# Kernel tuning notes

Measured on AMD Instinct MI355X. Metric: run time of the kernel, lower is better.

## Reference

```python
import jax, jax.numpy as jnp
import numpy as np

H = 64          # hiddens_dims
K = 3           # Chebyshev order
B = 16          # graphs in batch
NPG = 16384     # nodes per graph
N = B * NPG     # total nodes
E = 2_097_152   # total edges
R = 2191        # num_residues (hard-coded in source)
E_REF = R * 16
HALF = N // 2   # backbone count == sidechain count (mask is balanced per graph)


def _lin(k, fan_in, shape):
    return jax.random.uniform(k, shape, jnp.float32, -1.0, 1.0) / np.sqrt(fan_in)


def setup_inputs() -> dict:
    key = jax.random.key(0)
    ks = jax.random.split(key, 40)
    inp = {}
    inp["x"] = jax.random.normal(ks[0], (N, 3), jnp.float32)
    inp["edge_index"] = jax.random.randint(ks[1], (2, E), 0, N)
    inp["batch"] = jnp.repeat(jnp.arange(B, dtype=jnp.int32), NPG)
    blk = jnp.concatenate([jnp.ones((NPG // 2,), bool), jnp.zeros((NPG // 2,), bool)])
    inp["mask"] = jnp.tile(blk, B)  # backbone=True first half of each graph block
    inp["x_ref"] = jax.random.normal(ks[2], (R, 3), jnp.float32)
    inp["edgeref"] = jax.random.randint(ks[3], (2, E_REF), 0, R)
    i = 4
    for name, cin in [("cw0", 3), ("cw1", H), ("cw2", H), ("rw0", 3), ("rw1", H), ("rw2", H)]:
        inp[name] = _lin(ks[i], cin, (K, cin, H)); i += 1
        inp[name.replace("w", "b")] = jnp.zeros((H,), jnp.float32)  # ChebConv bias init = zeros
    for name, cin, cout in [("mlp_w", 2 * H, H), ("mlpP2_w", 2 * H, H),
                            ("rep0_w", H, H), ("rep1_w", H, H), ("rep2_w", H, 3)]:
        inp[name] = _lin(ks[i], cin, (cin, cout)); i += 1
        inp[name.replace("_w", "_b")] = _lin(ks[i], cin, (cout,)); i += 1
    return inp


def cheb_conv(x, edge_index, W, b, n):
    # PyG ChebConv with sym normalization, lambda_max=2: L_hat = -D^-1/2 A D^-1/2 (diag = 0)
    row, col = edge_index[0], edge_index[1]
    deg = jax.ops.segment_sum(jnp.ones_like(x[:, 0])[row] * 0 + 1.0, row, num_segments=n)
    dinv = jnp.where(deg > 0, jax.lax.rsqrt(jnp.maximum(deg, 1e-12)), 0.0)
    w = -(dinv[row] * dinv[col])  # [E]

    def prop(h):  # L_hat @ h via gather + segment_sum
        return jax.ops.segment_sum(w[:, None] * h[col], row, num_segments=n)

    Tx0 = x
    out = Tx0 @ W[0]
    Tx1 = prop(x)
    out = out + Tx1 @ W[1]
    for k in range(2, K):
        Tx2 = 2.0 * prop(Tx1) - Tx0
        out = out + Tx2 @ W[k]
        Tx0, Tx1 = Tx1, Tx2
    return out + b


def _forward(x, edge_index, mask, x_ref, edgeref,
             cw0, cb0, cw1, cb1, cw2, cb2, rw0, rb0, rw1, rb1, rw2, rb2,
             mlp_w, mlp_b, mlpP2_w, mlpP2_b,
             rep0_w, rep0_b, rep1_w, rep1_b, rep2_w, rep2_b):
    # main GNN stack (tanh after all but last; dropout is identity in eval)
    h = jnp.tanh(cheb_conv(x, edge_index, cw0, cb0, N))
    h = jnp.tanh(cheb_conv(h, edge_index, cw1, cb1, N))
    h = cheb_conv(h, edge_index, cw2, cb2, N)

    bb_idx = jnp.nonzero(mask, size=HALF)[0]
    sc_idx = jnp.nonzero(~mask, size=HALF)[0]
    x_bb = h[bb_idx].reshape(B, -1, H).mean(axis=1)[:, None, :]  # [B,1,H]
    x_sc = h[sc_idx].reshape(B, -1, H).mean(axis=1)[:, None, :]  # [B,1,H]

    # reference-graph stack: source bug makes `conv2 != self.convs[-1]` always True,
    # so tanh follows every convRef layer
    r = jnp.tanh(cheb_conv(x_ref, edgeref, rw0, rb0, R))
    r = jnp.tanh(cheb_conv(r, edgeref, rw1, rb1, R))
    r = jnp.tanh(cheb_conv(r, edgeref, rw2, rb2, R))
    r = jnp.broadcast_to(r[None], (B, R, H))

    bb_rep = jnp.broadcast_to(x_bb, (B, R, H))
    phase1 = jnp.concatenate([r, bb_rep], axis=-1) @ mlp_w + mlp_b        # [B,R,H]
    sc_rep = jnp.broadcast_to(x_sc, (B, R, H))
    phase2 = jnp.concatenate([phase1, sc_rep], axis=-1) @ mlpP2_w + mlpP2_b  # [B,R,H]

    res = phase2.reshape(-1, H)
    res = jax.nn.relu(res @ rep0_w + rep0_b)
    res = jax.nn.relu(res @ rep1_w + rep1_b)
    res = jax.nn.relu(res @ rep2_w + rep2_b)  # [B*R, 3]
    return res.reshape(-1, 3), x_bb, x_sc


def reference(x, edge_index, batch, mask, x_ref, edgeref,
              cw0, cb0, cw1, cb1, cw2, cb2, rw0, rb0, rw1, rb1, rw2, rb2,
              mlp_w, mlp_b, mlpP2_w, mlpP2_b,
              rep0_w, rep0_b, rep1_w, rep1_b, rep2_w, rep2_b):
    del batch  # only used for len(batch.unique()) == B, a static constant here
    return _forward(x, edge_index, mask, x_ref, edgeref,
                    cw0, cb0, cw1, cb1, cw2, cb2, rw0, rb0, rw1, rb1, rw2, rb2,
                    mlp_w, mlp_b, mlpP2_w, mlpP2_b,
                    rep0_w, rep0_b, rep1_w, rep1_b, rep2_w, rep2_b)
```

## Files before the change

### kernel.cpp

```cpp
#include <hip/hip_runtime.h>
#include <hip/hip_fp16.h>
#include <math.h>

#define NN 262144
#define NE 2097152
#define RR 2191
#define ER (RR*16)
#define NB 16
#define BRR (NB*RR)
#define OUT_RES (BRR*3)

typedef __attribute__((ext_vector_type(8))) _Float16 half8;
typedef __attribute__((ext_vector_type(4))) float f32x4;

__global__ void k_hist(const int* __restrict__ row, int* __restrict__ deg, int nE){
  int i = blockIdx.x*blockDim.x + threadIdx.x;
  int st = gridDim.x*blockDim.x;
  for (; i < nE; i += st) atomicAdd(&deg[row[i]], 1);
}

__global__ void k_scan1(const int* __restrict__ deg, int* __restrict__ rowptr,
                        int* __restrict__ partials, float* __restrict__ dinv){
  __shared__ int s[256];
  int t = threadIdx.x; int i = blockIdx.x*256 + t;
  int v = deg[i]; s[t] = v; __syncthreads();
  dinv[i] = v > 0 ? 1.0f/sqrtf((float)v) : 0.0f;
  for (int off = 1; off < 256; off <<= 1){
    int x = (t >= off) ? s[t-off] : 0; __syncthreads();
    s[t] += x; __syncthreads();
  }
  rowptr[i] = s[t] - v;
  if (t == 255) partials[blockIdx.x] = s[255];
}

__global__ void k_scan2(int* __restrict__ partials){
  __shared__ int s[1024];
  int t = threadIdx.x; int v = partials[t]; s[t] = v; __syncthreads();
  for (int off = 1; off < 1024; off <<= 1){
    int x = (t >= off) ? s[t-off] : 0; __syncthreads();
    s[t] += x; __syncthreads();
  }
  partials[t] = s[t] - v;
}

__global__ void k_scan3(int* __restrict__ rowptr, const int* __restrict__ partials){
  int t = threadIdx.x; int i = blockIdx.x*256 + t;
  rowptr[i] += partials[blockIdx.x];
  if (i == 0) rowptr[NN] = NE;
}

__global__ void k_scan_small(const int* __restrict__ deg, int* __restrict__ rowptr,
                             float* __restrict__ dinv, int n){
  __shared__ int s[256];
  int t = threadIdx.x;
  int carry = 0;
  for (int base = 0; base < n; base += 256){
    int idx = base + t;
    int v = (idx < n) ? deg[idx] : 0;
    if (idx < n) dinv[idx] = v > 0 ? 1.0f/sqrtf((float)v) : 0.0f;
    s[t] = v; __syncthreads();
    for (int off = 1; off < 256; off <<= 1){
      int x = (t >= off) ? s[t-off] : 0; __syncthreads();
      s[t] += x; __syncthreads();
    }
    if (idx < n) rowptr[idx] = carry + s[t] - v;
    carry += s[255];
    __syncthreads();
  }
  if (t == 0) rowptr[n] = carry;
}

__global__ void k_scatter(const int* __restrict__ row, const int* __restrict__ col,
                          const float* __restrict__ dinv, const int* __restrict__ rowptr,
                          int* __restrict__ cursor, int2* __restrict__ pair, int nE){
  int i = blockIdx.x*blockDim.x + threadIdx.x;
  int st = gridDim.x*blockDim.x;
  for (; i < nE; i += st){
    int r = row[i], c = col[i];
    int pos = rowptr[r] + atomicAdd(&cursor[r], 1);
    pair[pos] = make_int2(c, __float_as_int(-dinv[r]*dinv[c]));
  }
}

__global__ void k_pad3(const float* __restrict__ src, float4* __restrict__ dst, int n){
  int i = blockIdx.x*blockDim.x + threadIdx.x;
  if (i < n) dst[i] = make_float4(src[i*3], src[i*3+1], src[i*3+2], 0.0f);
}

__global__ void k_prop3p(const float4* __restrict__ h, float4* __restrict__ y,
                         const int* __restrict__ rowptr, const int2* __restrict__ pair, int n){
  int i = blockIdx.x*blockDim.x + threadIdx.x;
  if (i >= n) return;
  float a0 = 0.f, a1 = 0.f, a2 = 0.f;
  int s = rowptr[i], e = rowptr[i+1];
  int p = s;
  for (; p + 4 <= e; p += 4){
    int2 q0 = pair[p], q1 = pair[p+1], q2 = pair[p+2], q3 = pair[p+3];
    float4 v0 = h[q0.x], v1 = h[q1.x], v2 = h[q2.x], v3 = h[q3.x];
    float w0 = __int_as_float(q0.y), w1 = __int_as_float(q1.y);
    float w2 = __int_as_float(q2.y), w3 = __int_as_float(q3.y);
    a0 = fmaf(w0,v0.x, fmaf(w1,v1.x, fmaf(w2,v2.x, fmaf(w3,v3.x, a0))));
    a1 = fmaf(w0,v0.y, fmaf(w1,v1.y, fmaf(w2,v2.y, fmaf(w3,v3.y, a1))));
    a2 = fmaf(w0,v0.z, fmaf(w1,v1.z, fmaf(w2,v2.z, fmaf(w3,v3.z, a2))));
  }
  for (; p < e; p++){
    int2 q = pair[p]; float wv = __int_as_float(q.y);
    float4 v = h[q.x];
    a0 = fmaf(wv, v.x, a0); a1 = fmaf(wv, v.y, a1); a2 = fmaf(wv, v.z, a2);
  }
  y[i] = make_float4(a0, a1, a2, 0.0f);
}

__global__ void k_prop64(const float* __restrict__ h, float* __restrict__ y,
                         const int* __restrict__ rowptr, const int2* __restrict__ pair, int n){
  int t = threadIdx.x, lane = t & 63;
  int i = blockIdx.x*4 + (t >> 6);
  if (i >= n) return;
  float acc = 0.f;
  int s = rowptr[i], e = rowptr[i+1];
  int p = s;
  for (; p + 4 <= e; p += 4){
    int2 q0 = pair[p], q1 = pair[p+1], q2 = pair[p+2], q3 = pair[p+3];
    float v0 = h[(size_t)q0.x*64 + lane], v1 = h[(size_t)q1.x*64 + lane];
    float v2 = h[(size_t)q2.x*64 + lane], v3 = h[(size_t)q3.x*64 + lane];
    acc = fmaf(__int_as_float(q0.y),v0, fmaf(__int_as_float(q1.y),v1,
          fmaf(__int_as_float(q2.y),v2, fmaf(__int_as_float(q3.y),v3, acc))));
  }
  for (; p < e; p++){
    int2 q = pair[p];
    acc = fmaf(__int_as_float(q.y), h[(size_t)q.x*64 + lane], acc);
  }
  y[(size_t)i*64 + lane] = acc;
}

__global__ void __launch_bounds__(256) k_prop64h(
    const uint4* __restrict__ h4, uint4* __restrict__ y4,
    const int* __restrict__ rowptr, const int2* __restrict__ pair, int n){
  int t = threadIdx.x;
  int sub = t & 7;
  int row = blockIdx.x*32 + (t >> 3);
  if (row >= n) return;
  int s = rowptr[row], e = rowptr[row+1];
  float ac[8];
  #pragma unroll
  for (int k = 0; k < 8; k++) ac[k] = 0.f;
  int p = s;
  for (; p + 8 <= e; p += 8){
    int2 q[8]; uint4 v[8];
    #pragma unroll
    for (int j = 0; j < 8; j++) q[j] = pair[p+j];
    #pragma unroll
    for (int j = 0; j < 8; j++) v[j] = h4[(size_t)q[j].x*8 + sub];
    #pragma unroll
    for (int j = 0; j < 8; j++){
      float wv = __int_as_float(q[j].y);
      #pragma unroll
      for (int k = 0; k < 4; k++){
        float2 f = __half22float2(((const __half2*)&v[j])[k]);
        ac[2*k]   = fmaf(wv, f.x, ac[2*k]);
        ac[2*k+1] = fmaf(wv, f.y, ac[2*k+1]);
      }
    }
  }
  for (; p + 4 <= e; p += 4){
    int2 q[4]; uint4 v[4];
    #pragma unroll
    for (int j = 0; j < 4; j++) q[j] = pair[p+j];
    #pragma unroll
    for (int j = 0; j < 4; j++) v[j] = h4[(size_t)q[j].x*8 + sub];
    #pragma unroll
    for (int j = 0; j < 4; j++){
      float wv = __int_as_float(q[j].y);
      #pragma unroll
      for (int k = 0; k < 4; k++){
        float2 f = __half22float2(((const __half2*)&v[j])[k]);
        ac[2*k]   = fmaf(wv, f.x, ac[2*k]);
        ac[2*k+1] = fmaf(wv, f.y, ac[2*k+1]);
      }
    }
  }
  for (; p < e; p++){
    int2 q = pair[p];
    float wv = __int_as_float(q.y);
    uint4 v = h4[(size_t)q.x*8 + sub];
    #pragma unroll
    for (int k = 0; k < 4; k++){
      float2 f = __half22float2(((const __half2*)&v)[k]);
      ac[2*k]   = fmaf(wv, f.x, ac[2*k]);
      ac[2*k+1] = fmaf(wv, f.y, ac[2*k+1]);
    }
  }
  uint4 r;
  #pragma unroll
  for (int k = 0; k < 4; k++){
    __half2 hp = __floats2half2_rn(ac[2*k], ac[2*k+1]);
    ((unsigned*)&r)[k] = *(unsigned*)&hp;
  }
  y4[(size_t)row*8 + sub] = r;
}

__global__ void k_combine3f(const float4* __restrict__ x, const float4* __restrict__ t1,
                            const float4* __restrict__ t2, const float* __restrict__ W,
                            const float* __restrict__ bias, float* __restrict__ out, int n){
  int t = threadIdx.x, lane = t & 63;
  int i = blockIdx.x*4 + (t >> 6);
  if (i >= n) return;
  float4 px = x[i], p1 = t1[i], p2 = t2[i];
  const float* fx = (const float*)&px;
  const float* f1 = (const float*)&p1;
  const float* f2 = (const float*)&p2;
  float acc = bias[lane];
  #pragma unroll
  for (int j = 0; j < 3; j++){
    float x0 = fx[j], x1 = f1[j];
    float x2 = 2.0f*f2[j] - x0;
    acc += x0*W[      j*64 + lane]
         + x1*W[192 + j*64 + lane]
         + x2*W[384 + j*64 + lane];
  }
  out[(size_t)i*64 + lane] = tanhf(acc);
}

__global__ void k_combine3h(const float4* __restrict__ x, const float4* __restrict__ t1,
                            const float4* __restrict__ t2, const float* __restrict__ W,
                            const float* __restrict__ bias, __half* __restrict__ out, int n){
  int t = threadIdx.x, lane = t & 63;
  int i = blockIdx.x*4 + (t >> 6);
  if (i >= n) return;
  float4 px = x[i], p1 = t1[i], p2 = t2[i];
  const float* fx = (const float*)&px;
  const float* f1 = (const float*)&p1;
  const float* f2 = (const float*)&p2;
  float acc = bias[lane];
  #pragma unroll
  for (int j = 0; j < 3; j++){
    float x0 = fx[j], x1 = f1[j];
    float x2 = 2.0f*f2[j] - x0;
    acc += x0*W[      j*64 + lane]
         + x1*W[192 + j*64 + lane]
         + x2*W[384 + j*64 + lane];
  }
  out[(size_t)i*64 + lane] = __float2half_rn(tanhf(acc));
}

__global__ void k_weff(const float* __restrict__ W, float* __restrict__ D){
  int i = blockIdx.x*blockDim.x + threadIdx.x;
  D[i]        = W[i] - W[8192 + i];
  D[4096 + i] = W[4096 + i];
  D[8192 + i] = 2.0f * W[8192 + i];
}

__global__ void k_wpack(const float* __restrict__ W, _Float16* __restrict__ D){
  int t = blockIdx.x*blockDim.x + threadIdx.x;
  int reg = t & 7, lane = (t >> 3) & 63, nt = (t >> 9) & 3, kc = t >> 11;
  int m = kc >> 1;
  int kin = (kc & 1)*32 + ((lane >> 4) & 3)*8 + reg;
  int n = nt*16 + (lane & 15);
  float eff;
  if      (m == 0) eff = W[kin*64 + n] - W[8192 + kin*64 + n];
  else if (m == 1) eff = W[4096 + kin*64 + n];
  else             eff = 2.0f * W[8192 + kin*64 + n];
  D[t] = (_Float16)eff;
}

__global__ void __launch_bounds__(256) k_combine64m(
    const __half* A, const __half* B, const __half* C,
    const _Float16* __restrict__ wfrag, const float* __restrict__ bias,
    __half* out, int ntiles, int wavestride){
  int t = threadIdx.x;
  int lane = t & 63;
  int wv = blockIdx.x*4 + (t >> 6);
  half8 bf[24];
  #pragma unroll
  for (int i = 0; i < 24; i++)
    bf[i] = *(const half8*)(wfrag + ((size_t)(i*64 + lane))*8);
  int col = lane & 15, grp = (lane >> 4) & 3;
  float b0 = bias[col], b1 = bias[16+col], b2 = bias[32+col], b3 = bias[48+col];
  for (int tile = wv; tile < ntiles; tile += wavestride){
    size_t rb = (size_t)tile*16;
    f32x4 acc0 = {b0,b0,b0,b0}, acc1 = {b1,b1,b1,b1};
    f32x4 acc2 = {b2,b2,b2,b2}, acc3 = {b3,b3,b3,b3};
    #pragma unroll
    for (int kc = 0; kc < 6; kc++){
      const __half* s = (kc < 2) ? A : (kc < 4) ? B : C;
      half8 a = *(const half8*)(s + (rb + col)*64 + (kc & 1)*32 + grp*8);
      acc0 = __builtin_amdgcn_mfma_f32_16x16x32_f16(a, bf[kc*4+0], acc0, 0,0,0);
      acc1 = __builtin_amdgcn_mfma_f32_16x16x32_f16(a, bf[kc*4+1], acc1, 0,0,0);
      acc2 = __builtin_amdgcn_mfma_f32_16x16x32_f16(a, bf[kc*4+2], acc2, 0,0,0);
      acc3 = __builtin_amdgcn_mfma_f32_16x16x32_f16(a, bf[kc*4+3], acc3, 0,0,0);
    }
    __half* o = out + (rb + grp*4)*64;
    #pragma unroll
    for (int r = 0; r < 4; r++){
      o[(size_t)r*64 +      col] = __float2half_rn(tanhf(acc0[r]));
      o[(size_t)r*64 + 16 + col] = __float2half_rn(tanhf(acc1[r]));
      o[(size_t)r*64 + 32 + col] = __float2half_rn(tanhf(acc2[r]));
      o[(size_t)r*64 + 48 + col] = __float2half_rn(tanhf(acc3[r]));
    }
  }
}

__global__ void k_pool3(const __half2* __restrict__ hA, const __half2* __restrict__ hB,
                        const __half2* __restrict__ hC, float* __restrict__ pA,
                        float* __restrict__ pB, float* __restrict__ pC){
  const __half2* src = (blockIdx.y == 0) ? hA : (blockIdx.y == 1) ? hB : hC;
  float* dst         = (blockIdx.y == 0) ? pA : (blockIdx.y == 1) ? pB : pC;
  int blk = blockIdx.x;
  int chunk = blk & 15, seg = blk >> 4;
  int t = threadIdx.x, ch2 = t & 31, rsub = t >> 5;
  int base = seg*8192 + chunk*512;
  float ax = 0.f, ay = 0.f;
  for (int j = 0; j < 64; j++){
    int row = base + rsub + j*8;
    float2 v = __half22float2(src[(size_t)row*32 + ch2]);
    ax += v.x; ay += v.y;
  }
  __shared__ float sx[256], sy[256];
  sx[t] = ax; sy[t] = ay; __syncthreads();
  if (t < 32){
    float tx = 0.f, ty = 0.f;
    #pragma unroll
    for (int j = 0; j < 8; j++){ tx += sx[ch2 + j*32]; ty += sy[ch2 + j*32]; }
    int b = seg >> 1, half_ = seg & 1;
    atomicAdd(&dst[half_*1024 + b*64 + ch2*2],     tx);
    atomicAdd(&dst[half_*1024 + b*64 + ch2*2 + 1], ty);
  }
}

__global__ void k_combine_pooled(const float* __restrict__ pA, const float* __restrict__ pB,
                                 const float* __restrict__ pC, const float* __restrict__ weff,
                                 const float* __restrict__ bias, float* __restrict__ xbbsc,
                                 float* __restrict__ dout){
  int i = blockIdx.x*blockDim.x + threadIdx.x;
  int pr = i >> 6, c = i & 63;
  const float* a = pA + pr*64;
  const float* b = pB + pr*64;
  const float* cc = pC + pr*64;
  float v = 0.f;
  for (int k = 0; k < 64; k++){
    v = fmaf(a[k],  weff[        k*64 + c], v);
    v = fmaf(b[k],  weff[4096 +  k*64 + c], v);
    v = fmaf(cc[k], weff[8192 +  k*64 + c], v);
  }
  v = v*(1.0f/8192.0f) + bias[c];
  xbbsc[i] = v;
  dout[OUT_RES + i] = v;
}

__global__ void __launch_bounds__(256) k_combine64f(
    const float* __restrict__ A, const float* __restrict__ Bm, const float* __restrict__ C,
    const float* __restrict__ Weff, const float* __restrict__ bias,
    float* __restrict__ out, int n){
  int t = threadIdx.x;
  int lane = t & 63;
  int wid  = __builtin_amdgcn_readfirstlane(t >> 6);
  int half_ = wid & 1;
  int row  = blockIdx.x*128 + (wid >> 1)*64 + lane;
  bool active = (row < n);
  float acc[32];
  #pragma unroll
  for (int c = 0; c < 32; c++) acc[c] = bias[half_*32 + c];
  if (active){
    #pragma unroll 1
    for (int m = 0; m < 3; m++){
      const float* src = (m == 0 ? A : (m == 1 ? Bm : C)) + (size_t)row*64;
      const float* Wm  = Weff + m*4096 + half_*32;
      #pragma unroll 1
      for (int k4 = 0; k4 < 16; k4++){
        float4 a4 = *(const float4*)(src + k4*4);
        const float* wk = Wm + k4*256;
        #pragma unroll
        for (int kk = 0; kk < 4; kk++){
          float a = (kk == 0) ? a4.x : (kk == 1) ? a4.y : (kk == 2) ? a4.z : a4.w;
          #pragma unroll
          for (int c = 0; c < 32; c++)
            acc[c] = fmaf(a, wk[kk*64 + c], acc[c]);
        }
      }
    }
  }
  __syncthreads();
  if (active){
    float* o = out + (size_t)row*64 + half_*32;
    #pragma unroll
    for (int c = 0; c < 32; c++) o[c] = tanhf(acc[c]);
  }
}

__global__ void k_refchain(const float* __restrict__ refA, const float* __restrict__ mlp_w,
                           const float* __restrict__ mlp2_w, const float* __restrict__ rep0_w,
                           float* __restrict__ rt3a, int n){
  int t = threadIdx.x, lane = t & 63;
  int i = blockIdx.x*4 + (t >> 6);
  if (i >= n) return;
  float v = refA[i*64 + lane];
  float a = 0.f;
  #pragma unroll
  for (int k = 0; k < 64; k++) a += __shfl(v, k, 64) * mlp_w[k*64 + lane];
  float b = 0.f;
  #pragma unroll
  for (int k = 0; k < 64; k++) b += __shfl(a, k, 64) * mlp2_w[k*64 + lane];
  float c = 0.f;
  #pragma unroll
  for (int k = 0; k < 64; k++) c += __shfl(b, k, 64) * rep0_w[k*64 + lane];
  rt3a[i*64 + lane] = c;
}

__global__ void k_bbchain(const float* __restrict__ xbbsc,
                          const float* __restrict__ mlp_w,  const float* __restrict__ mlp_b,
                          const float* __restrict__ mlp2_w, const float* __restrict__ mlp2_b,
                          const float* __restrict__ rep0_w, const float* __restrict__ rep0_b,
                          float* __restrict__ bt3a){
  int t = threadIdx.x, lane = t & 63;
  int i = blockIdx.x*4 + (t >> 6);
  if (i >= NB) return;
  float vbb = xbbsc[i*64 + lane];
  float vsc = xbbsc[1024 + i*64 + lane];
  float a = mlp_b[lane];
  #pragma unroll
  for (int k = 0; k < 64; k++) a += __shfl(vbb, k, 64) * mlp_w[4096 + k*64 + lane];
  float b = mlp2_b[lane];
  #pragma unroll
  for (int k = 0; k < 64; k++) b += __shfl(a, k, 64) * mlp2_w[k*64 + lane];
  #pragma unroll
  for (int k = 0; k < 64; k++) b += __shfl(vsc, k, 64) * mlp2_w[4096 + k*64 + lane];
  float c = rep0_b[lane];
  #pragma unroll
  for (int k = 0; k < 64; k++) c += __shfl(b, k, 64) * rep0_w[k*64 + lane];
  bt3a[i*64 + lane] = c;
}

__global__ void k_final(const float* __restrict__ rt3, const float* __restrict__ bt3,
                        const float* __restrict__ W1, const float* __restrict__ b1,
                        const float* __restrict__ W2, const float* __restrict__ b2,
                        float* __restrict__ dout){
  int t = threadIdx.x, lane = t & 63;
  int g = blockIdx.x*4 + (t >> 6);
  if (g >= BRR) return;
  int b = g / RR, r = g - b*RR;
  float m = rt3[r*64 + lane] + bt3[b*64 + lane];
  m = fmaxf(m, 0.0f);
  float acc = b1[lane];
  #pragma unroll
  for (int k = 0; k < 64; k++) acc += __shfl(m, k, 64) * W1[k*64 + lane];
  float u = fmaxf(acc, 0.0f);
  float p0 = u*W2[lane*3+0], p1 = u*W2[lane*3+1], p2 = u*W2[lane*3+2];
  #pragma unroll
  for (int off = 32; off > 0; off >>= 1){
    p0 += __shfl_xor(p0, off, 64);
    p1 += __shfl_xor(p1, off, 64);
    p2 += __shfl_xor(p2, off, 64);
  }
  if (lane == 0){
    dout[g*3+0] = fmaxf(p0 + b2[0], 0.0f);
    dout[g*3+1] = fmaxf(p1 + b2[1], 0.0f);
    dout[g*3+2] = fmaxf(p2 + b2[2], 0.0f);
  }
}

extern "C" void kernel_launch(void* const* d_in, const int* in_sizes, int n_in,
                              void* d_out, int out_size, void* d_ws, size_t ws_size,
                              hipStream_t stream){
  const float* x     = (const float*)d_in[0];
  const int*   eidx  = (const int*)d_in[1];
  const float* x_ref = (const float*)d_in[4];
  const int*   eref  = (const int*)d_in[5];
  const float* cw0 = (const float*)d_in[6],  *cb0 = (const float*)d_in[7];
  const float* cw1 = (const float*)d_in[8],  *cb1 = (const float*)d_in[9];
  const float* cw2 = (const float*)d_in[10], *cb2 = (const float*)d_in[11];
  const float* rw0 = (const float*)d_in[12], *rb0 = (const float*)d_in[13];
  const float* rw1 = (const float*)d_in[14], *rb1 = (const float*)d_in[15];
  const float* rw2 = (const float*)d_in[16], *rb2 = (const float*)d_in[17];
  const float* mlp_w  = (const float*)d_in[18], *mlp_b  = (const float*)d_in[19];
  const float* mlp2_w = (const float*)d_in[20], *mlp2_b = (const float*)d_in[21];
  const float* rep0_w = (const float*)d_in[22], *rep0_b = (const float*)d_in[23];
  const float* rep1_w = (const float*)d_in[24], *rep1_b = (const float*)d_in[25];
  const float* rep2_w = (const float*)d_in[26], *rep2_b = (const float*)d_in[27];
  float* out = (float*)d_out;

  char* w = (char*)d_ws;
  size_t off = 0;
  auto alloc = [&](size_t bytes)->void*{
    void* p = w + off;
    off = (off + bytes + 255) & ~(size_t)255;
    return p;
  };
  int*   deg     = (int*)  alloc(NN*4);
  int*   cursor  = (int*)  alloc(NN*4);
  int*   degR    = (int*)  alloc(RR*4);
  int*   cursorR = (int*)  alloc(RR*4);
  float* poolA   = (float*)alloc(2048*4);
  float* poolB   = (float*)alloc(2048*4);
  float* poolC   = (float*)alloc(2048*4);
  size_t zero_bytes = off;

  int*   rowptr   = (int*)  alloc((NN+1)*4);
  int*   partials = (int*)  alloc(1024*4);
  int*   rowptrR  = (int*)  alloc((RR+1)*4);
  float* dinv     = (float*)alloc(NN*4);
  float* dinvR    = (float*)alloc(RR*4);
  int2*  cpair    = (int2*) alloc((size_t)NE*8);
  int2*  cpairR   = (int2*) alloc((size_t)ER*8);
  float4* x4      = (float4*)alloc((size_t)NN*16);
  float4* t1_4    = (float4*)alloc((size_t)NN*16);
  float4* t2_4    = (float4*)alloc((size_t)NN*16);
  float4* xr4     = (float4*)alloc((size_t)RR*16);
  float4* rt1_4   = (float4*)alloc((size_t)RR*16);
  float4* rt2_4   = (float4*)alloc((size_t)RR*16);
  __half* hA      = (__half*)alloc((size_t)NN*64*2);
  __half* hB      = (__half*)alloc((size_t)NN*64*2);
  __half* hC      = (__half*)alloc((size_t)NN*64*2);
  float* refA     = (float*)alloc(RR*64*4);
  float* refB     = (float*)alloc(RR*64*4);
  float* refC     = (float*)alloc(RR*64*4);
  float* xbbsc    = (float*)alloc(2048*4);
  float* rt3a     = (float*)alloc(RR*64*4);
  float* bt3a     = (float*)alloc(NB*64*4);
  float* weffC2   = (float*)alloc(12288*4);
  float* weffR1   = (float*)alloc(12288*4);
  float* weffR2   = (float*)alloc(12288*4);
  _Float16* wfragC1 = (_Float16*)alloc(12288*2);
  (void)ws_size; (void)in_sizes; (void)n_in; (void)out_size;

  hipMemsetAsync(d_ws, 0, zero_bytes, stream);

  k_weff<<<16, 256, 0, stream>>>(cw2, weffC2);
  k_weff<<<16, 256, 0, stream>>>(rw1, weffR1);
  k_weff<<<16, 256, 0, stream>>>(rw2, weffR2);
  k_wpack<<<48, 256, 0, stream>>>(cw1, wfragC1);
  k_pad3<<<1024, 256, 0, stream>>>(x, x4, NN);
  k_pad3<<<9, 256, 0, stream>>>(x_ref, xr4, RR);

  k_hist<<<2048, 256, 0, stream>>>(eidx, deg, NE);
  k_hist<<<64,   256, 0, stream>>>(eref, degR, ER);
  k_scan1<<<1024, 256, 0, stream>>>(deg, rowptr, partials, dinv);
  k_scan2<<<1, 1024, 0, stream>>>(partials);
  k_scan3<<<1024, 256, 0, stream>>>(rowptr, partials);
  k_scan_small<<<1, 256, 0, stream>>>(degR, rowptrR, dinvR, RR);
  k_scatter<<<2048, 256, 0, stream>>>(eidx, eidx+NE, dinv, rowptr, cursor, cpair, NE);
  k_scatter<<<64,   256, 0, stream>>>(eref, eref+ER, dinvR, rowptrR, cursorR, cpairR, ER);

  k_prop3p<<<1024, 256, 0, stream>>>(x4, t1_4, rowptr, cpair, NN);
  k_prop3p<<<1024, 256, 0, stream>>>(t1_4, t2_4, rowptr, cpair, NN);
  k_combine3h<<<NN/4, 256, 0, stream>>>(x4, t1_4, t2_4, cw0, cb0, hA, NN);
  k_prop64h<<<NN/32, 256, 0, stream>>>((const uint4*)hA, (uint4*)hB, rowptr, cpair, NN);
  k_prop64h<<<NN/32, 256, 0, stream>>>((const uint4*)hB, (uint4*)hC, rowptr, cpair, NN);
  k_combine64m<<<1024, 256, 0, stream>>>(hA, hB, hC, wfragC1, cb1, hA, NN/16, 4096);
  k_prop64h<<<NN/32, 256, 0, stream>>>((const uint4*)hA, (uint4*)hB, rowptr, cpair, NN);
  k_prop64h<<<NN/32, 256, 0, stream>>>((const uint4*)hB, (uint4*)hC, rowptr, cpair, NN);
  k_pool3<<<dim3(512,3), 256, 0, stream>>>((const __half2*)hA, (const __half2*)hB,
                                           (const __half2*)hC, poolA, poolB, poolC);
  k_combine_pooled<<<8, 256, 0, stream>>>(poolA, poolB, poolC, weffC2, cb2, xbbsc, out);

  k_prop3p<<<9, 256, 0, stream>>>(xr4, rt1_4, rowptrR, cpairR, RR);
  k_prop3p<<<9, 256, 0, stream>>>(rt1_4, rt2_4, rowptrR, cpairR, RR);
  k_combine3f<<<548, 256, 0, stream>>>(xr4, rt1_4, rt2_4, rw0, rb0, refA, RR);
  k_prop64<<<548, 256, 0, stream>>>(refA, refB, rowptrR, cpairR, RR);
  k_prop64<<<548, 256, 0, stream>>>(refB, refC, rowptrR, cpairR, RR);
  k_combine64f<<<(RR+127)/128, 256, 0, stream>>>(refA, refB, refC, weffR1, rb1, refA, RR);
  k_prop64<<<548, 256, 0, stream>>>(refA, refB, rowptrR, cpairR, RR);
  k_prop64<<<548, 256, 0, stream>>>(refB, refC, rowptrR, cpairR, RR);
  k_combine64f<<<(RR+127)/128, 256, 0, stream>>>(refA, refB, refC, weffR2, rb2, refA, RR);

  k_refchain<<<548, 256, 0, stream>>>(refA, mlp_w, mlp2_w, rep0_w, rt3a, RR);
  k_bbchain<<<4, 256, 0, stream>>>(xbbsc, mlp_w, mlp_b, mlp2_w, mlp2_b, rep0_w, rep0_b, bt3a);

  k_final<<<(BRR+3)/4, 256, 0, stream>>>(rt3a, bt3a, rep1_w, rep1_b, rep2_w, rep2_b, out);
}
```

Measured before the change: 769.9 us.

## Record per-edge rank during histogram and fuse preprocessing kernels into fewer launches

The histogram pass now stores each edge's atomic return value as a byte rank, so the CSR scatter computes its slot as rowptr plus rank and no longer needs a second atomic pass over a cursor array. The main-graph and reference-graph histogram, scan and scatter kernels are merged into shared launches, and the six weight and padding prep kernels become one 2D-grid kernel. The scatter also uses nontemporal stores. This cuts launch count and atomic traffic, but it assumes every node degree fits in a byte, adds a rank buffer write and read, and the edge order within a row now follows histogram atomic order.

```diff
diff --git a/kernel.cpp b/kernel.cpp
--- a/kernel.cpp
+++ b/kernel.cpp
@@ -13,10 +13,22 @@
 typedef __attribute__((ext_vector_type(8))) _Float16 half8;
 typedef __attribute__((ext_vector_type(4))) float f32x4;
 
-__global__ void k_hist(const int* __restrict__ row, int* __restrict__ deg, int nE){
-  int i = blockIdx.x*blockDim.x + threadIdx.x;
-  int st = gridDim.x*blockDim.x;
-  for (; i < nE; i += st) atomicAdd(&deg[row[i]], 1);
+__global__ void k_hist2(const int* __restrict__ eM, int* __restrict__ degM,
+                        unsigned char* __restrict__ rankM,
+                        const int* __restrict__ eR, int* __restrict__ degR,
+                        unsigned char* __restrict__ rankR){
+  int b = blockIdx.x;
+  if (b < 2048){
+    for (int i = b*256 + threadIdx.x; i < NE; i += 2048*256){
+      int old = atomicAdd(&degM[eM[i]], 1);
+      rankM[i] = (unsigned char)old;
+    }
+  } else {
+    for (int i = (b-2048)*256 + threadIdx.x; i < ER; i += 64*256){
+      int old = atomicAdd(&degR[eR[i]], 1);
+      rankR[i] = (unsigned char)old;
+    }
+  }
 }
 
 __global__ void k_scan1(const int* __restrict__ deg, int* __restrict__ rowptr,
@@ -33,14 +45,36 @@
   if (t == 255) partials[blockIdx.x] = s[255];
 }
 
-__global__ void k_scan2(int* __restrict__ partials){
+__global__ void __launch_bounds__(1024) k_scan2m(int* __restrict__ partials,
+                                                 const int* __restrict__ degR,
+                                                 int* __restrict__ rowptrR,
+                                                 float* __restrict__ dinvR){
   __shared__ int s[1024];
-  int t = threadIdx.x; int v = partials[t]; s[t] = v; __syncthreads();
-  for (int off = 1; off < 1024; off <<= 1){
-    int x = (t >= off) ? s[t-off] : 0; __syncthreads();
-    s[t] += x; __syncthreads();
-  }
-  partials[t] = s[t] - v;
+  int t = threadIdx.x;
+  if (blockIdx.x == 0){
+    int v = partials[t]; s[t] = v; __syncthreads();
+    for (int off = 1; off < 1024; off <<= 1){
+      int x = (t >= off) ? s[t-off] : 0; __syncthreads();
+      s[t] += x; __syncthreads();
+    }
+    partials[t] = s[t] - v;
+  } else {
+    int carry = 0;
+    for (int base = 0; base < RR; base += 1024){
+      int idx = base + t;
+      int v = (idx < RR) ? degR[idx] : 0;
+      if (idx < RR) dinvR[idx] = v > 0 ? 1.0f/sqrtf((float)v) : 0.0f;
+      s[t] = v; __syncthreads();
+      for (int off = 1; off < 1024; off <<= 1){
+        int x = (t >= off) ? s[t-off] : 0; __syncthreads();
+        s[t] += x; __syncthreads();
+      }
+      if (idx < RR) rowptrR[idx] = carry + s[t] - v;
+      carry += s[1023];
+      __syncthreads();
+    }
+    if (t == 0) rowptrR[RR] = carry;
+  }
 }
 
 __global__ void k_scan3(int* __restrict__ rowptr, const int* __restrict__ partials){
@@ -49,42 +83,65 @@
   if (i == 0) rowptr[NN] = NE;
 }
 
-__global__ void k_scan_small(const int* __restrict__ deg, int* __restrict__ rowptr,
-                             float* __restrict__ dinv, int n){
-  __shared__ int s[256];
-  int t = threadIdx.x;
-  int carry = 0;
-  for (int base = 0; base < n; base += 256){
-    int idx = base + t;
-    int v = (idx < n) ? deg[idx] : 0;
-    if (idx < n) dinv[idx] = v > 0 ? 1.0f/sqrtf((float)v) : 0.0f;
-    s[t] = v; __syncthreads();
-    for (int off = 1; off < 256; off <<= 1){
-      int x = (t >= off) ? s[t-off] : 0; __syncthreads();
-      s[t] += x; __syncthreads();
-    }
-    if (idx < n) rowptr[idx] = carry + s[t] - v;
-    carry += s[255];
-    __syncthreads();
-  }
-  if (t == 0) rowptr[n] = carry;
-}
-
-__global__ void k_scatter(const int* __restrict__ row, const int* __restrict__ col,
-                          const float* __restrict__ dinv, const int* __restrict__ rowptr,
-                          int* __restrict__ cursor, int2* __restrict__ pair, int nE){
+__global__ void k_scatter2(const int* __restrict__ eM, const float* __restrict__ dinv,
+                           const int* __restrict__ rowptr, const unsigned char* __restrict__ rankM,
+                           int2* __restrict__ pair,
+                           const int* __restrict__ eR, const float* __restrict__ dinvR,
+                           const int* __restrict__ rowptrR, const unsigned char* __restrict__ rankR,
+                           int2* __restrict__ pairR){
+  int b = blockIdx.x;
+  if (b < 2048){
+    for (int i = b*256 + threadIdx.x; i < NE; i += 2048*256){
+      int r = eM[i], c = eM[NE + i];
+      int pos = rowptr[r] + rankM[i];
+      unsigned wbits = (unsigned)__float_as_int(-dinv[r]*dinv[c]);
+      long long v = (unsigned)c | ((long long)wbits << 32);
+      __builtin_nontemporal_store(v, (long long*)(pair + pos));
+    }
+  } else {
+    for (int i = (b-2048)*256 + threadIdx.x; i < ER; i += 64*256){
+      int r = eR[i], c = eR[ER + i];
+      int pos = rowptrR[r] + rankR[i];
+      unsigned wbits = (unsigned)__float_as_int(-dinvR[r]*dinvR[c]);
+      long long v = (unsigned)c | ((long long)wbits << 32);
+      __builtin_nontemporal_store(v, (long long*)(pairR + pos));
+    }
+  }
+}
+
+__global__ void k_prep(const float* __restrict__ cw1, const float* __restrict__ cw2,
+                       const float* __restrict__ rw1, const float* __restrict__ rw2,
+                       float* __restrict__ weffC2, float* __restrict__ weffR1,
+                       float* __restrict__ weffR2, _Float16* __restrict__ wfragC1,
+                       const float* __restrict__ x, float4* __restrict__ x4,
+                       const float* __restrict__ x_ref, float4* __restrict__ xr4){
+  int y = blockIdx.y;
   int i = blockIdx.x*blockDim.x + threadIdx.x;
-  int st = gridDim.x*blockDim.x;
-  for (; i < nE; i += st){
-    int r = row[i], c = col[i];
-    int pos = rowptr[r] + atomicAdd(&cursor[r], 1);
-    pair[pos] = make_int2(c, __float_as_int(-dinv[r]*dinv[c]));
-  }
-}
-
-__global__ void k_pad3(const float* __restrict__ src, float4* __restrict__ dst, int n){
-  int i = blockIdx.x*blockDim.x + threadIdx.x;
-  if (i < n) dst[i] = make_float4(src[i*3], src[i*3+1], src[i*3+2], 0.0f);
+  if (y < 3){
+    if (i < 4096){
+      const float* W = (y == 0) ? cw2 : (y == 1) ? rw1 : rw2;
+      float* D       = (y == 0) ? weffC2 : (y == 1) ? weffR1 : weffR2;
+      D[i]        = W[i] - W[8192 + i];
+      D[4096 + i] = W[4096 + i];
+      D[8192 + i] = 2.0f * W[8192 + i];
+    }
+  } else if (y == 3){
+    if (i < 12288){
+      int reg = i & 7, lane = (i >> 3) & 63, nt = (i >> 9) & 3, kc = i >> 11;
+      int m = kc >> 1;
+      int kin = (kc & 1)*32 + ((lane >> 4) & 3)*8 + reg;
+      int n = nt*16 + (lane & 15);
+      float eff;
+      if      (m == 0) eff = cw1[kin*64 + n] - cw1[8192 + kin*64 + n];
+      else if (m == 1) eff = cw1[4096 + kin*64 + n];
+      else             eff = 2.0f * cw1[8192 + kin*64 + n];
+      wfragC1[i] = (_Float16)eff;
+    }
+  } else if (y == 4){
+    if (i < NN) x4[i] = make_float4(x[i*3], x[i*3+1], x[i*3+2], 0.0f);
+  } else {
+    if (i < RR) xr4[i] = make_float4(x_ref[i*3], x_ref[i*3+1], x_ref[i*3+2], 0.0f);
+  }
 }
 
 __global__ void k_prop3p(const float4* __restrict__ h, float4* __restrict__ y,
@@ -241,26 +298,6 @@
          + x2*W[384 + j*64 + lane];
   }
   out[(size_t)i*64 + lane] = __float2half_rn(tanhf(acc));
-}
-
-__global__ void k_weff(const float* __restrict__ W, float* __restrict__ D){
-  int i = blockIdx.x*blockDim.x + threadIdx.x;
-  D[i]        = W[i] - W[8192 + i];
-  D[4096 + i] = W[4096 + i];
-  D[8192 + i] = 2.0f * W[8192 + i];
-}
-
-__global__ void k_wpack(const float* __restrict__ W, _Float16* __restrict__ D){
-  int t = blockIdx.x*blockDim.x + threadIdx.x;
-  int reg = t & 7, lane = (t >> 3) & 63, nt = (t >> 9) & 3, kc = t >> 11;
-  int m = kc >> 1;
-  int kin = (kc & 1)*32 + ((lane >> 4) & 3)*8 + reg;
-  int n = nt*16 + (lane & 15);
-  float eff;
-  if      (m == 0) eff = W[kin*64 + n] - W[8192 + kin*64 + n];
-  else if (m == 1) eff = W[4096 + kin*64 + n];
-  else             eff = 2.0f * W[8192 + kin*64 + n];
-  D[t] = (_Float16)eff;
 }
 
 __global__ void __launch_bounds__(256) k_combine64m(
@@ -486,9 +523,7 @@
     return p;
   };
   int*   deg     = (int*)  alloc(NN*4);
-  int*   cursor  = (int*)  alloc(NN*4);
   int*   degR    = (int*)  alloc(RR*4);
-  int*   cursorR = (int*)  alloc(RR*4);
   float* poolA   = (float*)alloc(2048*4);
   float* poolB   = (float*)alloc(2048*4);
   float* poolC   = (float*)alloc(2048*4);
@@ -499,6 +534,8 @@
   int*   rowptrR  = (int*)  alloc((RR+1)*4);
   float* dinv     = (float*)alloc(NN*4);
   float* dinvR    = (float*)alloc(RR*4);
+  unsigned char* rankM = (unsigned char*)alloc(NE);
+  unsigned char* rankR = (unsigned char*)alloc(ER);
   int2*  cpair    = (int2*) alloc((size_t)NE*8);
   int2*  cpairR   = (int2*) alloc((size_t)ER*8);
   float4* x4      = (float4*)alloc((size_t)NN*16);
@@ -524,21 +561,16 @@
 
   hipMemsetAsync(d_ws, 0, zero_bytes, stream);
 
-  k_weff<<<16, 256, 0, stream>>>(cw2, weffC2);
-  k_weff<<<16, 256, 0, stream>>>(rw1, weffR1);
-  k_weff<<<16, 256, 0, stream>>>(rw2, weffR2);
-  k_wpack<<<48, 256, 0, stream>>>(cw1, wfragC1);
-  k_pad3<<<1024, 256, 0, stream>>>(x, x4, NN);
-  k_pad3<<<9, 256, 0, stream>>>(x_ref, xr4, RR);
-
-  k_hist<<<2048, 256, 0, stream>>>(eidx, deg, NE);
-  k_hist<<<64,   256, 0, stream>>>(eref, degR, ER);
+  k_prep<<<dim3(1024, 6), 256, 0, stream>>>(cw1, cw2, rw1, rw2,
+                                            weffC2, weffR1, weffR2, wfragC1,
+                                            x, x4, x_ref, xr4);
+
+  k_hist2<<<2112, 256, 0, stream>>>(eidx, deg, rankM, eref, degR, rankR);
   k_scan1<<<1024, 256, 0, stream>>>(deg, rowptr, partials, dinv);
-  k_scan2<<<1, 1024, 0, stream>>>(partials);
+  k_scan2m<<<2, 1024, 0, stream>>>(partials, degR, rowptrR, dinvR);
   k_scan3<<<1024, 256, 0, stream>>>(rowptr, partials);
-  k_scan_small<<<1, 256, 0, stream>>>(degR, rowptrR, dinvR, RR);
-  k_scatter<<<2048, 256, 0, stream>>>(eidx, eidx+NE, dinv, rowptr, cursor, cpair, NE);
-  k_scatter<<<64,   256, 0, stream>>>(eref, eref+ER, dinvR, rowptrR, cursorR, cpairR, ER);
+  k_scatter2<<<2112, 256, 0, stream>>>(eidx, dinv, rowptr, rankM, cpair,
+                                       eref, dinvR, rowptrR, rankR, cpairR);
 
   k_prop3p<<<1024, 256, 0, stream>>>(x4, t1_4, rowptr, cpair, NN);
   k_prop3p<<<1024, 256, 0, stream>>>(t1_4, t2_4, rowptr, cpair, NN);
```

Result: faster. 724.1 us (-5.9%).
